# Kernel tuning notes

Measured on AMD Instinct MI355X. Metric: run time of the kernel, lower is better.

## Reference

```python
import jax, jax.numpy as jnp
import numpy as np

N_NODES = 100000
N_EDGES = 1600000
IN_C = 128
HID_C = 32
HEADS = 4
OUT_C = 40
N_GRAPHS = 64
NEG_SLOPE = 0.2  # PyG GATConv default


def setup_inputs() -> dict:
    key = jax.random.key(0)
    ks = jax.random.split(key, 12)
    x = jax.random.normal(ks[0], (N_NODES, IN_C), dtype=jnp.float32)
    edge_index = jax.random.randint(ks[1], (2, N_EDGES), 0, N_NODES, dtype=jnp.int64)
    batch = jnp.sort(jax.random.randint(ks[2], (N_NODES,), 0, N_GRAPHS, dtype=jnp.int64))
    s1 = 1.0 / np.sqrt(IN_C)
    s2 = 1.0 / np.sqrt(HEADS * HID_C)
    W1 = jax.random.normal(ks[3], (IN_C, HEADS * HID_C), dtype=jnp.float32) * s1
    a1_src = jax.random.normal(ks[4], (HEADS, HID_C), dtype=jnp.float32) * s1
    a1_dst = jax.random.normal(ks[5], (HEADS, HID_C), dtype=jnp.float32) * s1
    b1 = jnp.zeros((HEADS * HID_C,), dtype=jnp.float32)
    W2 = jax.random.normal(ks[6], (HEADS * HID_C, OUT_C), dtype=jnp.float32) * s2
    a2_src = jax.random.normal(ks[7], (1, OUT_C), dtype=jnp.float32) * s2
    a2_dst = jax.random.normal(ks[8], (1, OUT_C), dtype=jnp.float32) * s2
    b2 = jnp.zeros((OUT_C,), dtype=jnp.float32)
    return {"x": x, "edge_index": edge_index, "batch": batch,
            "W1": W1, "a1_src": a1_src, "a1_dst": a1_dst, "b1": b1,
            "W2": W2, "a2_src": a2_src, "a2_dst": a2_dst, "b2": b2}


def gat_conv(x, src, dst, W, a_src, a_dst, bias, heads, out_c, concat):
    """PyG-style GATConv (eval mode, self-loops included in src/dst)."""
    N = x.shape[0]
    h = (x @ W).reshape(N, heads, out_c)              # [N,H,C]
    alpha_s = jnp.einsum('nhc,hc->nh', h, a_src)      # [N,H]
    alpha_d = jnp.einsum('nhc,hc->nh', h, a_dst)
    e = alpha_s[src] + alpha_d[dst]                   # [E,H]
    e = jnp.where(e > 0, e, NEG_SLOPE * e)            # LeakyReLU(0.2)
    # segment softmax over edges grouped by destination node
    m = jax.ops.segment_max(e, dst, num_segments=N)   # [N,H]
    ex = jnp.exp(e - m[dst])
    denom = jax.ops.segment_sum(ex, dst, num_segments=N)
    alpha = ex / (denom[dst] + 1e-16)                 # [E,H]
    msg = h[src] * alpha[..., None]                   # [E,H,C]
    out = jax.ops.segment_sum(msg, dst, num_segments=N)  # [N,H,C]
    if concat:
        out = out.reshape(N, heads * out_c)
    else:
        out = out.mean(axis=1)
    return out + bias


def reference(x, edge_index, batch, W1, a1_src, a1_dst, b1, W2, a2_src, a2_dst, b2):
    N = x.shape[0]
    # add self-loops (PyG GATConv default add_self_loops=True)
    loop = jnp.arange(N, dtype=edge_index.dtype)
    src = jnp.concatenate([edge_index[0], loop])
    dst = jnp.concatenate([edge_index[1], loop])
    h = gat_conv(x, src, dst, W1, a1_src, a1_dst, b1, HEADS, HID_C, concat=True)
    h = jax.nn.elu(h)
    h = gat_conv(h, src, dst, W2, a2_src, a2_dst, b2, 1, OUT_C, concat=False)
    # global mean pool over graphs
    sums = jax.ops.segment_sum(h, batch, num_segments=N_GRAPHS)
    counts = jax.ops.segment_sum(jnp.ones((N,), dtype=h.dtype), batch, num_segments=N_GRAPHS)
    return sums / jnp.maximum(counts, 1.0)[:, None]
```

## Files before the change

kernel.cpp:

```cpp
#include <hip/hip_runtime.h>

#define NNODES 100000
#define NEDGES 1600000
#define ETOT   1700000
#define NGRAPH 64
#define NEG    0.2f
#define NB_SCAN 98
#define NPART  8
#define DPP    12500
#define SCAT_BPP 128
#define SCAT_CH  ((ETOT + SCAT_BPP - 1) / SCAT_BPP)
#define PCH    1024
#define NHB    1661
#define NGB    1563

using f32x2 = __attribute__((ext_vector_type(2))) float;

__device__ __forceinline__ float f4get(const float4& v, int j) {
    return j == 0 ? v.x : j == 1 ? v.y : j == 2 ? v.z : v.w;
}

__device__ __forceinline__ unsigned short f2bf(float f) {
    unsigned u = __float_as_uint(f);
    u = (u + 0x7fffu + ((u >> 16) & 1u)) >> 16;
    return (unsigned short)u;
}
__device__ __forceinline__ float bf_lo(unsigned u) { return __uint_as_float(u << 16); }
__device__ __forceinline__ float bf_hi(unsigned u) { return __uint_as_float(u & 0xffff0000u); }

__global__ __launch_bounds__(256, 4) void k_fused1(const int* __restrict__ ei,
        int* __restrict__ cnt, int* __restrict__ rank,
        const float* __restrict__ x, const float* __restrict__ W1,
        const float* __restrict__ a1s, const float* __restrict__ a1d,
        unsigned* __restrict__ h1q, float* __restrict__ as1, float* __restrict__ ad1) {
    __shared__ float sX[64 * 128];
    int bid = blockIdx.x;
    if (bid & 1) {
        int hb = bid >> 1;
        int base = hb * 1024 + threadIdx.x;
        int e0 = base, e1 = base + 256, e2 = base + 512, e3 = base + 768;
        bool v0 = e0 < ETOT, v1 = e1 < ETOT, v2 = e2 < ETOT, v3 = e3 < ETOT;
        int d0 = 0, d1 = 0, d2 = 0, d3 = 0;
        if (v0) d0 = (e0 < NEDGES) ? ei[NEDGES + e0] : e0 - NEDGES;
        if (v1) d1 = (e1 < NEDGES) ? ei[NEDGES + e1] : e1 - NEDGES;
        if (v2) d2 = (e2 < NEDGES) ? ei[NEDGES + e2] : e2 - NEDGES;
        if (v3) d3 = (e3 < NEDGES) ? ei[NEDGES + e3] : e3 - NEDGES;
        int r0 = 0, r1 = 0, r2 = 0, r3 = 0;
        if (v0) r0 = atomicAdd(&cnt[d0], 1);
        if (v1) r1 = atomicAdd(&cnt[d1], 1);
        if (v2) r2 = atomicAdd(&cnt[d2], 1);
        if (v3) r3 = atomicAdd(&cnt[d3], 1);
        if (v0) rank[e0] = r0;
        if (v1) rank[e1] = r1;
        if (v2) rank[e2] = r2;
        if (v3) rank[e3] = r3;
        return;
    }
    int gb = bid >> 1;
    if (gb >= NGB) return;
    int t = threadIdx.x;
    int nbase = gb * 64;
    int nrows = NNODES - nbase; if (nrows > 64) nrows = 64;
    {
        const float4* X4 = (const float4*)(x + (size_t)nbase * 128);
        float4* sX4 = (float4*)sX;
        for (int i = t; i < nrows * 32; i += 256) sX4[i] = X4[i];
    }
    __syncthreads();

    int colg = t & 31, rowg = t >> 5;
    int c0 = colg * 4, n0 = rowg * 8;
    float acc[8][4];
#pragma unroll
    for (int i = 0; i < 8; ++i)
        acc[i][0] = acc[i][1] = acc[i][2] = acc[i][3] = 0.f;

    for (int k = 0; k < 128; k += 4) {
        float4 w0 = *(const float4*)&W1[(size_t)(k + 0) * 128 + c0];
        float4 w1 = *(const float4*)&W1[(size_t)(k + 1) * 128 + c0];
        float4 w2 = *(const float4*)&W1[(size_t)(k + 2) * 128 + c0];
        float4 w3 = *(const float4*)&W1[(size_t)(k + 3) * 128 + c0];
#pragma unroll
        for (int i = 0; i < 8; ++i) {
            float4 xv = *(const float4*)&sX[(n0 + i) * 128 + k];
            acc[i][0] = fmaf(xv.x, w0.x, acc[i][0]); acc[i][1] = fmaf(xv.x, w0.y, acc[i][1]);
            acc[i][2] = fmaf(xv.x, w0.z, acc[i][2]); acc[i][3] = fmaf(xv.x, w0.w, acc[i][3]);
            acc[i][0] = fmaf(xv.y, w1.x, acc[i][0]); acc[i][1] = fmaf(xv.y, w1.y, acc[i][1]);
            acc[i][2] = fmaf(xv.y, w1.z, acc[i][2]); acc[i][3] = fmaf(xv.y, w1.w, acc[i][3]);
            acc[i][0] = fmaf(xv.z, w2.x, acc[i][0]); acc[i][1] = fmaf(xv.z, w2.y, acc[i][1]);
            acc[i][2] = fmaf(xv.z, w2.z, acc[i][2]); acc[i][3] = fmaf(xv.z, w2.w, acc[i][3]);
            acc[i][0] = fmaf(xv.w, w3.x, acc[i][0]); acc[i][1] = fmaf(xv.w, w3.y, acc[i][1]);
            acc[i][2] = fmaf(xv.w, w3.z, acc[i][2]); acc[i][3] = fmaf(xv.w, w3.w, acc[i][3]);
        }
    }

    int head = colg >> 3;
    float ws0 = a1s[c0], ws1 = a1s[c0 + 1], ws2 = a1s[c0 + 2], ws3 = a1s[c0 + 3];
    float wd0 = a1d[c0], wd1 = a1d[c0 + 1], wd2 = a1d[c0 + 2], wd3 = a1d[c0 + 3];
#pragma unroll
    for (int i = 0; i < 8; ++i) {
        int n = n0 + i;
        float ps = acc[i][0] * ws0 + acc[i][1] * ws1 + acc[i][2] * ws2 + acc[i][3] * ws3;
        float pd = acc[i][0] * wd0 + acc[i][1] * wd1 + acc[i][2] * wd2 + acc[i][3] * wd3;
        ps += __shfl_xor(ps, 1); ps += __shfl_xor(ps, 2); ps += __shfl_xor(ps, 4);
        pd += __shfl_xor(pd, 1); pd += __shfl_xor(pd, 2); pd += __shfl_xor(pd, 4);
        if (n < nrows) {
            int q = __builtin_amdgcn_cvt_pk_fp8_f32(acc[i][0], acc[i][1], 0, false);
            q = __builtin_amdgcn_cvt_pk_fp8_f32(acc[i][2], acc[i][3], q, true);
            h1q[((size_t)(nbase + n)) * 32 + colg] = (unsigned)q;
            if ((colg & 7) == 0) {
                as1[(size_t)(nbase + n) * 4 + head] = ps;
                ad1[(size_t)(nbase + n) * 4 + head] = pd;
            }
        }
    }
}

__global__ __launch_bounds__(256) void k_scan1(const int* __restrict__ cnt,
                                               int* __restrict__ excl,
                                               int* __restrict__ bsum) {
    __shared__ int tmp[256];
    int t = threadIdx.x;
    int base = blockIdx.x * 1024 + t * 4;
    int v0 = base + 0 < NNODES ? cnt[base + 0] : 0;
    int v1 = base + 1 < NNODES ? cnt[base + 1] : 0;
    int v2 = base + 2 < NNODES ? cnt[base + 2] : 0;
    int v3 = base + 3 < NNODES ? cnt[base + 3] : 0;
    int tot = v0 + v1 + v2 + v3;
    tmp[t] = tot;
    __syncthreads();
    for (int off = 1; off < 256; off <<= 1) {
        int x = (t >= off) ? tmp[t - off] : 0;
        __syncthreads();
        tmp[t] += x;
        __syncthreads();
    }
    int tbase = tmp[t] - tot;
    if (base + 0 < NNODES) excl[base + 0] = tbase;
    if (base + 1 < NNODES) excl[base + 1] = tbase + v0;
    if (base + 2 < NNODES) excl[base + 2] = tbase + v0 + v1;
    if (base + 3 < NNODES) excl[base + 3] = tbase + v0 + v1 + v2;
    if (t == 255) bsum[blockIdx.x] = tmp[255];
}

__global__ __launch_bounds__(256) void k_offs(const int* __restrict__ excl,
                                              const int* __restrict__ bsum,
                                              int* __restrict__ offs) {
    __shared__ int sp;
    int b = blockIdx.x, t = threadIdx.x;
    if (t == 0) {
        int p = 0;
        for (int i = 0; i < b; ++i) p += bsum[i];
        sp = p;
    }
    __syncthreads();
    int prefix = sp;
#pragma unroll
    for (int j = 0; j < 4; ++j) {
        int idx = b * 1024 + t * 4 + j;
        if (idx < NNODES) offs[idx] = excl[idx] + prefix;
    }
}

__global__ __launch_bounds__(256) void k_scatter(const int* __restrict__ ei,
                                                 const int* __restrict__ rank,
                                                 const int* __restrict__ offs,
                                                 int* __restrict__ csr_src) {
    int p = blockIdx.x & (NPART - 1);
    int chunk = blockIdx.x / NPART;
    int dlo = p * DPP, dhi = dlo + DPP;
    int e0 = chunk * SCAT_CH;
    int e1 = e0 + SCAT_CH; if (e1 > ETOT) e1 = ETOT;
    for (int e = e0 + threadIdx.x; e < e1; e += 1024) {
        int eA = e, eB = e + 256, eC = e + 512, eD = e + 768;
        bool vA = eA < e1, vB = eB < e1, vC = eC < e1, vD = eD < e1;
        int dA = -1, dB = -1, dC = -1, dD = -1;
        if (vA) dA = (eA < NEDGES) ? ei[NEDGES + eA] : eA - NEDGES;
        if (vB) dB = (eB < NEDGES) ? ei[NEDGES + eB] : eB - NEDGES;
        if (vC) dC = (eC < NEDGES) ? ei[NEDGES + eC] : eC - NEDGES;
        if (vD) dD = (eD < NEDGES) ? ei[NEDGES + eD] : eD - NEDGES;
        if (dA >= dlo && dA < dhi) {
            int s = (eA < NEDGES) ? ei[eA] : dA;
            csr_src[offs[dA] + rank[eA]] = s;
        }
        if (dB >= dlo && dB < dhi) {
            int s = (eB < NEDGES) ? ei[eB] : dB;
            csr_src[offs[dB] + rank[eB]] = s;
        }
        if (dC >= dlo && dC < dhi) {
            int s = (eC < NEDGES) ? ei[eC] : dC;
            csr_src[offs[dC] + rank[eC]] = s;
        }
        if (dD >= dlo && dD < dhi) {
            int s = (eD < NEDGES) ? ei[eD] : dD;
            csr_src[offs[dD] + rank[eD]] = s;
        }
    }
}

__global__ __launch_bounds__(256) void k_node1(const int* __restrict__ csr_src,
        const int* __restrict__ offs, const int* __restrict__ cnt,
        const unsigned* __restrict__ h1q,
        const float4* __restrict__ as1v, const float4* __restrict__ ad1v,
        unsigned* __restrict__ out1b) {
    __shared__ float4 exbuf[8][32];
    int t = threadIdx.x;
    int grp = t >> 5, lane = t & 31;
    int node = blockIdx.x * 8 + grp;
    if (node >= NNODES) return;
    int head = lane >> 3;
    int off = offs[node];
    int deg = cnt[node];
    float4 adv = ad1v[node];
    float4 dp = make_float4(0.f, 0.f, 0.f, 0.f);
    float4 acc = make_float4(0.f, 0.f, 0.f, 0.f);
    const float* exs = (const float*)&exbuf[grp][0];

    for (int base = 0; base < deg; base += 32) {
        int m = deg - base; if (m > 32) m = 32;
        int sv = 0;
        if (lane < m) {
            sv = csr_src[off + base + lane];
            float4 av = as1v[sv];
            float v; float4 e;
            v = av.x + adv.x; v = v > 0.f ? v : NEG * v; e.x = __expf(v);
            v = av.y + adv.y; v = v > 0.f ? v : NEG * v; e.y = __expf(v);
            v = av.z + adv.z; v = v > 0.f ? v : NEG * v; e.z = __expf(v);
            v = av.w + adv.w; v = v > 0.f ? v : NEG * v; e.w = __expf(v);
            exbuf[grp][lane] = e;
            dp.x += e.x; dp.y += e.y; dp.z += e.z; dp.w += e.w;
        }
        __builtin_amdgcn_wave_barrier();
        int i = 0;
        for (; i + 4 <= m; i += 4) {
            int s0 = __shfl(sv, i + 0, 32);
            int s1 = __shfl(sv, i + 1, 32);
            int s2 = __shfl(sv, i + 2, 32);
            int s3 = __shfl(sv, i + 3, 32);
            unsigned q0 = h1q[(size_t)s0 * 32 + lane];
            unsigned q1 = h1q[(size_t)s1 * 32 + lane];
            unsigned q2 = h1q[(size_t)s2 * 32 + lane];
            unsigned q3 = h1q[(size_t)s3 * 32 + lane];
            float a0 = exs[(i + 0) * 4 + head];
            float a1 = exs[(i + 1) * 4 + head];
            float a2 = exs[(i + 2) * 4 + head];
            float a3 = exs[(i + 3) * 4 + head];
            f32x2 lo, hi;
            lo = __builtin_amdgcn_cvt_pk_f32_fp8((int)q0, false);
            hi = __builtin_amdgcn_cvt_pk_f32_fp8((int)q0, true);
            acc.x = fmaf(lo.x, a0, acc.x); acc.y = fmaf(lo.y, a0, acc.y);
            acc.z = fmaf(hi.x, a0, acc.z); acc.w = fmaf(hi.y, a0, acc.w);
            lo = __builtin_amdgcn_cvt_pk_f32_fp8((int)q1, false);
            hi = __builtin_amdgcn_cvt_pk_f32_fp8((int)q1, true);
            acc.x = fmaf(lo.x, a1, acc.x); acc.y = fmaf(lo.y, a1, acc.y);
            acc.z = fmaf(hi.x, a1, acc.z); acc.w = fmaf(hi.y, a1, acc.w);
            lo = __builtin_amdgcn_cvt_pk_f32_fp8((int)q2, false);
            hi = __builtin_amdgcn_cvt_pk_f32_fp8((int)q2, true);
            acc.x = fmaf(lo.x, a2, acc.x); acc.y = fmaf(lo.y, a2, acc.y);
            acc.z = fmaf(hi.x, a2, acc.z); acc.w = fmaf(hi.y, a2, acc.w);
            lo = __builtin_amdgcn_cvt_pk_f32_fp8((int)q3, false);
            hi = __builtin_amdgcn_cvt_pk_f32_fp8((int)q3, true);
            acc.x = fmaf(lo.x, a3, acc.x); acc.y = fmaf(lo.y, a3, acc.y);
            acc.z = fmaf(hi.x, a3, acc.z); acc.w = fmaf(hi.y, a3, acc.w);
        }
        for (; i < m; ++i) {
            int s = __shfl(sv, i, 32);
            float a = exs[i * 4 + head];
            unsigned hq = h1q[(size_t)s * 32 + lane];
            f32x2 lo = __builtin_amdgcn_cvt_pk_f32_fp8((int)hq, false);
            f32x2 hi = __builtin_amdgcn_cvt_pk_f32_fp8((int)hq, true);
            acc.x = fmaf(lo.x, a, acc.x);
            acc.y = fmaf(lo.y, a, acc.y);
            acc.z = fmaf(hi.x, a, acc.z);
            acc.w = fmaf(hi.y, a, acc.w);
        }
        __builtin_amdgcn_wave_barrier();
    }
#pragma unroll
    for (int msk = 1; msk < 32; msk <<= 1) {
        dp.x += __shfl_xor(dp.x, msk, 32);
        dp.y += __shfl_xor(dp.y, msk, 32);
        dp.z += __shfl_xor(dp.z, msk, 32);
        dp.w += __shfl_xor(dp.w, msk, 32);
    }
    float inv = 1.f / f4get(dp, head);
    unsigned p0 = (unsigned)f2bf(acc.x * inv) | ((unsigned)f2bf(acc.y * inv) << 16);
    unsigned p1 = (unsigned)f2bf(acc.z * inv) | ((unsigned)f2bf(acc.w * inv) << 16);
    uint2 pk; pk.x = p0; pk.y = p1;
    *(uint2*)&out1b[(size_t)node * 64 + lane * 2] = pk;
}

__global__ __launch_bounds__(256) void k_gemm2(const unsigned* __restrict__ in_b,
                                               const float* __restrict__ W2,
                                               const float* __restrict__ b1,
                                               const float* __restrict__ a2s,
                                               const float* __restrict__ a2d,
                                               unsigned short* __restrict__ h2b,
                                               float* __restrict__ as2,
                                               float* __restrict__ ad2) {
    __shared__ float sW[128 * 40];
    __shared__ float sX[128 * 132];
    int t = threadIdx.x;
    for (int i = t; i < 128 * 40 / 4; i += 256) ((float4*)sW)[i] = ((const float4*)W2)[i];
    int nbase = blockIdx.x * 128;
    int nrows = NNODES - nbase; if (nrows > 128) nrows = 128;
    {
        const uint4* X4 = (const uint4*)(in_b + (size_t)nbase * 64);
        for (int i = t; i < nrows * 16; i += 256) {
            int row = i >> 4, c8 = i & 15;
            uint4 v = X4[i];
            float4 bb0 = *(const float4*)&b1[c8 * 8];
            float4 bb1 = *(const float4*)&b1[c8 * 8 + 4];
            float f0 = bf_lo(v.x) + bb0.x, f1 = bf_hi(v.x) + bb0.y;
            float f2 = bf_lo(v.y) + bb0.z, f3 = bf_hi(v.y) + bb0.w;
            float f4 = bf_lo(v.z) + bb1.x, f5 = bf_hi(v.z) + bb1.y;
            float f6 = bf_lo(v.w) + bb1.z, f7 = bf_hi(v.w) + bb1.w;
            f0 = f0 > 0.f ? f0 : __expf(f0) - 1.f;
            f1 = f1 > 0.f ? f1 : __expf(f1) - 1.f;
            f2 = f2 > 0.f ? f2 : __expf(f2) - 1.f;
            f3 = f3 > 0.f ? f3 : __expf(f3) - 1.f;
            f4 = f4 > 0.f ? f4 : __expf(f4) - 1.f;
            f5 = f5 > 0.f ? f5 : __expf(f5) - 1.f;
            f6 = f6 > 0.f ? f6 : __expf(f6) - 1.f;
            f7 = f7 > 0.f ? f7 : __expf(f7) - 1.f;
            float* sp = &sX[row * 132 + c8 * 8];
            *(float4*)sp       = make_float4(f0, f1, f2, f3);
            *(float4*)(sp + 4) = make_float4(f4, f5, f6, f7);
        }
    }
    __syncthreads();

    int colg = t & 7, nodeg = t >> 3;
    int c0 = colg * 5;
    float acc[4][5];
#pragma unroll
    for (int i = 0; i < 4; ++i)
#pragma unroll
        for (int c = 0; c < 5; ++c) acc[i][c] = 0.f;

    for (int k = 0; k < 128; k += 4) {
        float4 xv[4];
#pragma unroll
        for (int i = 0; i < 4; ++i)
            xv[i] = *(const float4*)&sX[(nodeg + 32 * i) * 132 + k];
#pragma unroll
        for (int j = 0; j < 4; ++j) {
            float w0 = sW[(k + j) * 40 + c0 + 0];
            float w1 = sW[(k + j) * 40 + c0 + 1];
            float w2 = sW[(k + j) * 40 + c0 + 2];
            float w3 = sW[(k + j) * 40 + c0 + 3];
            float w4 = sW[(k + j) * 40 + c0 + 4];
#pragma unroll
            for (int i = 0; i < 4; ++i) {
                float xs = f4get(xv[i], j);
                acc[i][0] = fmaf(xs, w0, acc[i][0]);
                acc[i][1] = fmaf(xs, w1, acc[i][1]);
                acc[i][2] = fmaf(xs, w2, acc[i][2]);
                acc[i][3] = fmaf(xs, w3, acc[i][3]);
                acc[i][4] = fmaf(xs, w4, acc[i][4]);
            }
        }
    }

    float ws0 = a2s[c0], ws1 = a2s[c0 + 1], ws2 = a2s[c0 + 2], ws3 = a2s[c0 + 3], ws4 = a2s[c0 + 4];
    float wd0 = a2d[c0], wd1 = a2d[c0 + 1], wd2 = a2d[c0 + 2], wd3 = a2d[c0 + 3], wd4 = a2d[c0 + 4];
#pragma unroll
    for (int i = 0; i < 4; ++i) {
        int n = nodeg + 32 * i;
        float ps = acc[i][0]*ws0 + acc[i][1]*ws1 + acc[i][2]*ws2 + acc[i][3]*ws3 + acc[i][4]*ws4;
        float pd = acc[i][0]*wd0 + acc[i][1]*wd1 + acc[i][2]*wd2 + acc[i][3]*wd3 + acc[i][4]*wd4;
        ps += __shfl_xor(ps, 1); ps += __shfl_xor(ps, 2); ps += __shfl_xor(ps, 4);
        pd += __shfl_xor(pd, 1); pd += __shfl_xor(pd, 2); pd += __shfl_xor(pd, 4);
        if (n < nrows) {
            unsigned short* hp = h2b + (size_t)(nbase + n) * 40 + c0;
#pragma unroll
            for (int c = 0; c < 5; ++c) hp[c] = f2bf(acc[i][c]);
            if (colg == 0) {
                as2[nbase + n] = ps;
                ad2[nbase + n] = pd;
            }
        }
    }
}

__global__ __launch_bounds__(256) void k_node2(const int* __restrict__ csr_src,
        const int* __restrict__ offs, const int* __restrict__ cnt,
        const unsigned short* __restrict__ h2b,
        const float* __restrict__ as2, const float* __restrict__ ad2,
        float* __restrict__ out2) {
    int t = threadIdx.x;
    int grp = t >> 4, lane = t & 15;
    int node = blockIdx.x * 16 + grp;
    if (node >= NNODES) return;
    int off = offs[node];
    int deg = cnt[node];
    float adv = ad2[node];
    float dp = 0.f;
    float4 acc = make_float4(0.f, 0.f, 0.f, 0.f);

    for (int base = 0; base < deg; base += 16) {
        int m = deg - base; if (m > 16) m = 16;
        int sv = 0; float ex = 0.f;
        if (lane < m) {
            sv = csr_src[off + base + lane];
            float v = as2[sv] + adv;
            v = v > 0.f ? v : NEG * v;
            ex = __expf(v);
            dp += ex;
        }
        int i = 0;
        for (; i + 4 <= m; i += 4) {
            int s0 = __shfl(sv, i + 0, 16);
            int s1 = __shfl(sv, i + 1, 16);
            int s2 = __shfl(sv, i + 2, 16);
            int s3 = __shfl(sv, i + 3, 16);
            float a0 = __shfl(ex, i + 0, 16);
            float a1 = __shfl(ex, i + 1, 16);
            float a2 = __shfl(ex, i + 2, 16);
            float a3 = __shfl(ex, i + 3, 16);
            if (lane < 10) {
                uint2 h0 = *(const uint2*)(h2b + (size_t)s0 * 40 + lane * 4);
                uint2 h1 = *(const uint2*)(h2b + (size_t)s1 * 40 + lane * 4);
                uint2 h2 = *(const uint2*)(h2b + (size_t)s2 * 40 + lane * 4);
                uint2 h3 = *(const uint2*)(h2b + (size_t)s3 * 40 + lane * 4);
                acc.x = fmaf(bf_lo(h0.x), a0, acc.x); acc.y = fmaf(bf_hi(h0.x), a0, acc.y);
                acc.z = fmaf(bf_lo(h0.y), a0, acc.z); acc.w = fmaf(bf_hi(h0.y), a0, acc.w);
                acc.x = fmaf(bf_lo(h1.x), a1, acc.x); acc.y = fmaf(bf_hi(h1.x), a1, acc.y);
                acc.z = fmaf(bf_lo(h1.y), a1, acc.z); acc.w = fmaf(bf_hi(h1.y), a1, acc.w);
                acc.x = fmaf(bf_lo(h2.x), a2, acc.x); acc.y = fmaf(bf_hi(h2.x), a2, acc.y);
                acc.z = fmaf(bf_lo(h2.y), a2, acc.z); acc.w = fmaf(bf_hi(h2.y), a2, acc.w);
                acc.x = fmaf(bf_lo(h3.x), a3, acc.x); acc.y = fmaf(bf_hi(h3.x), a3, acc.y);
                acc.z = fmaf(bf_lo(h3.y), a3, acc.z); acc.w = fmaf(bf_hi(h3.y), a3, acc.w);
            }
        }
        for (; i < m; ++i) {
            int s = __shfl(sv, i, 16);
            float a = __shfl(ex, i, 16);
            if (lane < 10) {
                uint2 hv = *(const uint2*)(h2b + (size_t)s * 40 + lane * 4);
                acc.x = fmaf(bf_lo(hv.x), a, acc.x);
                acc.y = fmaf(bf_hi(hv.x), a, acc.y);
                acc.z = fmaf(bf_lo(hv.y), a, acc.z);
                acc.w = fmaf(bf_hi(hv.y), a, acc.w);
            }
        }
    }
#pragma unroll
    for (int msk = 1; msk < 16; msk <<= 1) dp += __shfl_xor(dp, msk, 16);
    float inv = 1.f / dp;
    if (lane < 10) {
        float4 o; o.x = acc.x * inv; o.y = acc.y * inv; o.z = acc.z * inv; o.w = acc.w * inv;
        *(float4*)(out2 + (size_t)node * 40 + lane * 4) = o;
    }
}

__global__ __launch_bounds__(256) void k_pool1(const float* __restrict__ out2,
        const int* __restrict__ batch, float* __restrict__ partial) {
    int t = threadIdx.x;
    if (t >= 240) return;
    int r = t / 40, c = t - r * 40;
    int base = blockIdx.x * PCH;
    int end = base + PCH; if (end > NNODES) end = NNODES;
    float sum = 0.f; int gcur = -1;
    for (int n = base + r; n < end; n += 6) {
        int g = batch[n];
        if (g != gcur) {
            if (gcur >= 0) unsafeAtomicAdd(&partial[gcur * 40 + c], sum);
            gcur = g; sum = 0.f;
        }
        sum += out2[(size_t)n * 40 + c];
    }
    if (gcur >= 0) unsafeAtomicAdd(&partial[gcur * 40 + c], sum);
}

__global__ void k_pool2(const float* __restrict__ partial, const int* __restrict__ batch,
                        const float* __restrict__ b2, float* __restrict__ out) {
    int i = blockIdx.x * 256 + threadIdx.x;
    if (i >= NGRAPH * 40) return;
    int g = i / 40, c = i - g * 40;
    int lo, hi;
    { int a = 0, b = NNODES; while (a < b) { int m = (a + b) >> 1; if (batch[m] < g) a = m + 1; else b = m; } lo = a; }
    { int a = lo, b = NNODES; while (a < b) { int m = (a + b) >> 1; if (batch[m] < g + 1) a = m + 1; else b = m; } hi = a; }
    int cntg = hi - lo;
    out[i] = cntg > 0 ? partial[i] / (float)cntg + b2[c] : 0.f;
}

extern "C" void kernel_launch(void* const* d_in, const int* in_sizes, int n_in,
                              void* d_out, int out_size, void* d_ws, size_t ws_size,
                              hipStream_t stream) {
    const float* x    = (const float*)d_in[0];
    const int*   ei   = (const int*)d_in[1];
    const int*   batch= (const int*)d_in[2];
    const float* W1   = (const float*)d_in[3];
    const float* a1s  = (const float*)d_in[4];
    const float* a1d  = (const float*)d_in[5];
    const float* b1   = (const float*)d_in[6];
    const float* W2   = (const float*)d_in[7];
    const float* a2s  = (const float*)d_in[8];
    const float* a2d  = (const float*)d_in[9];
    const float* b2   = (const float*)d_in[10];
    float* out = (float*)d_out;

    int* cnt      = (int*)d_ws;
    float* partial= (float*)(cnt + NNODES);
    int* excl     = (int*)(partial + NGRAPH * 40);
    int* offs     = excl + NNODES;
    int* bsum     = offs + NNODES;
    int* rank     = bsum + 128;
    int* csr      = rank + ETOT;
    float* as1    = (float*)(csr + ETOT);
    float* ad1    = as1 + (size_t)NNODES * 4;
    unsigned* h1q = (unsigned*)(ad1 + (size_t)NNODES * 4);
    unsigned* out1b = h1q + (size_t)NNODES * 32;
    float* as2    = (float*)(out1b + (size_t)NNODES * 64);
    float* ad2    = as2 + NNODES;
    unsigned short* h2b = (unsigned short*)(ad2 + NNODES);
    float* out2   = (float*)(h2b + (size_t)NNODES * 40);

    hipMemsetAsync(d_ws, 0, ((size_t)NNODES + NGRAPH * 40) * sizeof(int), stream);

    k_fused1<<<2 * NHB, 256, 0, stream>>>(ei, cnt, rank, x, W1, a1s, a1d, h1q, as1, ad1);

    k_scan1<<<NB_SCAN, 256, 0, stream>>>(cnt, excl, bsum);
    k_offs<<<NB_SCAN, 256, 0, stream>>>(excl, bsum, offs);
    k_scatter<<<NPART * SCAT_BPP, 256, 0, stream>>>(ei, rank, offs, csr);

    k_node1<<<(NNODES + 7) / 8, 256, 0, stream>>>(csr, offs, cnt, h1q,
                                                  (const float4*)as1, (const float4*)ad1, out1b);

    k_gemm2<<<(NNODES + 127) / 128, 256, 0, stream>>>(out1b, W2, b1, a2s, a2d, h2b, as2, ad2);
    k_node2<<<(NNODES + 15) / 16, 256, 0, stream>>>(csr, offs, cnt, h2b, as2, ad2, out2);

    k_pool1<<<(NNODES + PCH - 1) / PCH, 256, 0, stream>>>(out2, batch, partial);
    k_pool2<<<(NGRAPH * 40 + 255) / 256, 256, 0, stream>>>(partial, batch, b2, out);
}
```

Before: 342.3 us.

## Pad degree counters and handle self-loops analytically in CSR build

```diff
diff --git a/kernel.cpp b/kernel.cpp
--- a/kernel.cpp
+++ b/kernel.cpp
@@ -9,10 +9,12 @@
 #define NPART  8
 #define DPP    12500
 #define SCAT_BPP 128
-#define SCAT_CH  ((ETOT + SCAT_BPP - 1) / SCAT_BPP)
+#define SCAT_CHR 12500
+#define DSL    98
 #define PCH    1024
-#define NHB    1661
+#define NHB    1563
 #define NGB    1563
+#define CSTR   16
 
 using f32x2 = __attribute__((ext_vector_type(2))) float;
 
@@ -27,6 +29,17 @@
 }
 __device__ __forceinline__ float bf_lo(unsigned u) { return __uint_as_float(u << 16); }
 __device__ __forceinline__ float bf_hi(unsigned u) { return __uint_as_float(u & 0xffff0000u); }
+
+__global__ __launch_bounds__(256) void k_init(int* __restrict__ cnt, float* __restrict__ partial) {
+    int t = threadIdx.x, b = blockIdx.x;
+#pragma unroll
+    for (int j = 0; j < 4; ++j) {
+        int idx = b * 1024 + t * 4 + j;
+        if (idx < NNODES) cnt[(size_t)idx * CSTR] = 1;
+    }
+    int pi = b * 256 + t;
+    if (pi < NGRAPH * 40) partial[pi] = 0.f;
+}
 
 __global__ __launch_bounds__(256, 4) void k_fused1(const int* __restrict__ ei,
         int* __restrict__ cnt, int* __restrict__ rank,
@@ -39,17 +52,17 @@
         int hb = bid >> 1;
         int base = hb * 1024 + threadIdx.x;
         int e0 = base, e1 = base + 256, e2 = base + 512, e3 = base + 768;
-        bool v0 = e0 < ETOT, v1 = e1 < ETOT, v2 = e2 < ETOT, v3 = e3 < ETOT;
+        bool v0 = e0 < NEDGES, v1 = e1 < NEDGES, v2 = e2 < NEDGES, v3 = e3 < NEDGES;
         int d0 = 0, d1 = 0, d2 = 0, d3 = 0;
-        if (v0) d0 = (e0 < NEDGES) ? ei[NEDGES + e0] : e0 - NEDGES;
-        if (v1) d1 = (e1 < NEDGES) ? ei[NEDGES + e1] : e1 - NEDGES;
-        if (v2) d2 = (e2 < NEDGES) ? ei[NEDGES + e2] : e2 - NEDGES;
-        if (v3) d3 = (e3 < NEDGES) ? ei[NEDGES + e3] : e3 - NEDGES;
+        if (v0) d0 = ei[NEDGES + e0];
+        if (v1) d1 = ei[NEDGES + e1];
+        if (v2) d2 = ei[NEDGES + e2];
+        if (v3) d3 = ei[NEDGES + e3];
         int r0 = 0, r1 = 0, r2 = 0, r3 = 0;
-        if (v0) r0 = atomicAdd(&cnt[d0], 1);
-        if (v1) r1 = atomicAdd(&cnt[d1], 1);
-        if (v2) r2 = atomicAdd(&cnt[d2], 1);
-        if (v3) r3 = atomicAdd(&cnt[d3], 1);
+        if (v0) r0 = atomicAdd(&cnt[(size_t)d0 * CSTR], 1);
+        if (v1) r1 = atomicAdd(&cnt[(size_t)d1 * CSTR], 1);
+        if (v2) r2 = atomicAdd(&cnt[(size_t)d2 * CSTR], 1);
+        if (v3) r3 = atomicAdd(&cnt[(size_t)d3 * CSTR], 1);
         if (v0) rank[e0] = r0;
         if (v1) rank[e1] = r1;
         if (v2) rank[e2] = r2;
@@ -122,10 +135,10 @@
     __shared__ int tmp[256];
     int t = threadIdx.x;
     int base = blockIdx.x * 1024 + t * 4;
-    int v0 = base + 0 < NNODES ? cnt[base + 0] : 0;
-    int v1 = base + 1 < NNODES ? cnt[base + 1] : 0;
-    int v2 = base + 2 < NNODES ? cnt[base + 2] : 0;
-    int v3 = base + 3 < NNODES ? cnt[base + 3] : 0;
+    int v0 = base + 0 < NNODES ? cnt[(size_t)(base + 0) * CSTR] : 0;
+    int v1 = base + 1 < NNODES ? cnt[(size_t)(base + 1) * CSTR] : 0;
+    int v2 = base + 2 < NNODES ? cnt[(size_t)(base + 2) * CSTR] : 0;
+    int v3 = base + 3 < NNODES ? cnt[(size_t)(base + 3) * CSTR] : 0;
     int tot = v0 + v1 + v2 + v3;
     tmp[t] = tot;
     __syncthreads();
@@ -169,32 +182,24 @@
     int p = blockIdx.x & (NPART - 1);
     int chunk = blockIdx.x / NPART;
     int dlo = p * DPP, dhi = dlo + DPP;
-    int e0 = chunk * SCAT_CH;
-    int e1 = e0 + SCAT_CH; if (e1 > ETOT) e1 = ETOT;
+    {
+        int d = dlo + chunk * DSL + threadIdx.x;
+        if (threadIdx.x < DSL && d < dhi) csr_src[offs[d]] = d;
+    }
+    int e0 = chunk * SCAT_CHR;
+    int e1 = e0 + SCAT_CHR; if (e1 > NEDGES) e1 = NEDGES;
     for (int e = e0 + threadIdx.x; e < e1; e += 1024) {
         int eA = e, eB = e + 256, eC = e + 512, eD = e + 768;
         bool vA = eA < e1, vB = eB < e1, vC = eC < e1, vD = eD < e1;
         int dA = -1, dB = -1, dC = -1, dD = -1;
-        if (vA) dA = (eA < NEDGES) ? ei[NEDGES + eA] : eA - NEDGES;
-        if (vB) dB = (eB < NEDGES) ? ei[NEDGES + eB] : eB - NEDGES;
-        if (vC) dC = (eC < NEDGES) ? ei[NEDGES + eC] : eC - NEDGES;
-        if (vD) dD = (eD < NEDGES) ? ei[NEDGES + eD] : eD - NEDGES;
-        if (dA >= dlo && dA < dhi) {
-            int s = (eA < NEDGES) ? ei[eA] : dA;
-            csr_src[offs[dA] + rank[eA]] = s;
-        }
-        if (dB >= dlo && dB < dhi) {
-            int s = (eB < NEDGES) ? ei[eB] : dB;
-            csr_src[offs[dB] + rank[eB]] = s;
-        }
-        if (dC >= dlo && dC < dhi) {
-            int s = (eC < NEDGES) ? ei[eC] : dC;
-            csr_src[offs[dC] + rank[eC]] = s;
-        }
-        if (dD >= dlo && dD < dhi) {
-            int s = (eD < NEDGES) ? ei[eD] : dD;
-            csr_src[offs[dD] + rank[eD]] = s;
-        }
+        if (vA) dA = ei[NEDGES + eA];
+        if (vB) dB = ei[NEDGES + eB];
+        if (vC) dC = ei[NEDGES + eC];
+        if (vD) dD = ei[NEDGES + eD];
+        if (dA >= dlo && dA < dhi) csr_src[offs[dA] + rank[eA]] = ei[eA];
+        if (dB >= dlo && dB < dhi) csr_src[offs[dB] + rank[eB]] = ei[eB];
+        if (dC >= dlo && dC < dhi) csr_src[offs[dC] + rank[eC]] = ei[eC];
+        if (dD >= dlo && dD < dhi) csr_src[offs[dD] + rank[eD]] = ei[eD];
     }
 }
 
@@ -210,7 +215,7 @@
     if (node >= NNODES) return;
     int head = lane >> 3;
     int off = offs[node];
-    int deg = cnt[node];
+    int deg = cnt[(size_t)node * CSTR];
     float4 adv = ad1v[node];
     float4 dp = make_float4(0.f, 0.f, 0.f, 0.f);
     float4 acc = make_float4(0.f, 0.f, 0.f, 0.f);
@@ -393,7 +398,7 @@
     int node = blockIdx.x * 16 + grp;
     if (node >= NNODES) return;
     int off = offs[node];
-    int deg = cnt[node];
+    int deg = cnt[(size_t)node * CSTR];
     float adv = ad2[node];
     float dp = 0.f;
     float4 acc = make_float4(0.f, 0.f, 0.f, 0.f);
@@ -502,12 +507,12 @@
     float* out = (float*)d_out;
 
     int* cnt      = (int*)d_ws;
-    float* partial= (float*)(cnt + NNODES);
+    float* partial= (float*)(cnt + (size_t)NNODES * CSTR);
     int* excl     = (int*)(partial + NGRAPH * 40);
     int* offs     = excl + NNODES;
     int* bsum     = offs + NNODES;
     int* rank     = bsum + 128;
-    int* csr      = rank + ETOT;
+    int* csr      = rank + NEDGES;
     float* as1    = (float*)(csr + ETOT);
     float* ad1    = as1 + (size_t)NNODES * 4;
     unsigned* h1q = (unsigned*)(ad1 + (size_t)NNODES * 4);
@@ -517,7 +522,7 @@
     unsigned short* h2b = (unsigned short*)(ad2 + NNODES);
     float* out2   = (float*)(h2b + (size_t)NNODES * 40);
 
-    hipMemsetAsync(d_ws, 0, ((size_t)NNODES + NGRAPH * 40) * sizeof(int), stream);
+    k_init<<<NB_SCAN, 256, 0, stream>>>(cnt, partial);
 
     k_fused1<<<2 * NHB, 256, 0, stream>>>(ei, cnt, rank, x, W1, a1s, a1d, h1q, as1, ad1);
 
```

Result: no change. 346.8 us (+1.3%).
